# Performance work log

Measured on AMD Instinct MI355X. Metric: run time of the kernel, lower is better.

Reference implementation:

```python
import jax, jax.numpy as jnp
import numpy as np

B, C, H, W = 16, 64, 128, 128
HEADS, DH = 4, 32
HID = HEADS * DH  # 128
EPS = 1e-5


def setup_inputs() -> dict:
    key = jax.random.key(0)
    ks = jax.random.split(key, 3)
    x = jax.random.normal(ks[0], (B, C, H, W), jnp.float32)
    w_qkv = jax.random.normal(ks[1], (3 * HID, C), jnp.float32) * 0.05  # 1x1 conv, no bias
    w_out = jax.random.normal(ks[2], (C, HID), jnp.float32) * 0.05     # 1x1 conv
    b_out = jnp.zeros((C,), jnp.float32)
    gamma = jnp.ones((C,), jnp.float32)   # BatchNorm weight
    beta = jnp.zeros((C,), jnp.float32)   # BatchNorm bias
    return {"x": x, "w_qkv": w_qkv, "w_out": w_out, "b_out": b_out,
            "gamma": gamma, "beta": beta}


def reference(x, w_qkv, w_out, b_out, gamma, beta):
    b, c, h, w = x.shape
    scale = DH ** (-0.5)
    # 1x1 conv to qkv: [b, 3*HID, h, w]
    qkv = jnp.einsum('bcxy,oc->boxy', x, w_qkv)
    q, k, v = jnp.split(qkv, 3, axis=1)

    def rearr(t):  # b (h d) x y -> b h x y d
        return t.reshape(b, HEADS, DH, h, w).transpose(0, 1, 3, 4, 2)

    q, k, v = rearr(q), rearr(k), rearr(v)
    q = jax.nn.softmax(q, axis=-1) * scale  # softmax over feature dim d
    k = jax.nn.softmax(k, axis=-1)
    # linear attention: sum over spatial positions first (O(hw*d*e))
    context = jnp.einsum('bhxyd,bhxye->bhde', k, v)
    out = jnp.einsum('bhde,bhxyd->bhxye', context, q)
    # b h x y e -> b (h e) x y
    out = out.transpose(0, 1, 4, 2, 3).reshape(b, HID, h, w)
    # 1x1 conv out projection
    out = jnp.einsum('bcxy,oc->boxy', out, w_out) + b_out[None, :, None, None]
    # BatchNorm2d (training-mode batch statistics, biased variance, eps=1e-5)
    mean = out.mean(axis=(0, 2, 3), keepdims=True)
    var = ((out - mean) ** 2).mean(axis=(0, 2, 3), keepdims=True)
    out = (out - mean) * jax.lax.rsqrt(var + EPS)
    return out * gamma[None, :, None, None] + beta[None, :, None, None]
```

## Files before the change

kernel.cpp:

```cpp
#include <hip/hip_runtime.h>

typedef __attribute__((ext_vector_type(8))) short bf16x8;
typedef __attribute__((ext_vector_type(4))) float f32x4;

#define SCALEQ 0.17677669529663687f
#define EPSV 1e-5f

__device__ inline unsigned short f2bf(float f) {
  unsigned int u = __float_as_uint(f);
  return (unsigned short)((u + 0x7FFFu + ((u >> 16) & 1u)) >> 16);
}
__device__ inline unsigned int pack2(float a, float b) {
  return (unsigned int)f2bf(a) | ((unsigned int)f2bf(b) << 16);
}

__global__ __launch_bounds__(256) void kwconv(const float* __restrict__ wqkv,
                                              unsigned short* __restrict__ wbf) {
  const int i = blockIdx.x * 256 + threadIdx.x;
  const float4 v = *(const float4*)&wqkv[i * 4];
  *(uint2*)&wbf[i * 4] = make_uint2(pack2(v.x, v.y), pack2(v.z, v.w));
}

__global__ __launch_bounds__(256) void ktr(const float* __restrict__ x,
                                           unsigned short* __restrict__ xsw) {
  __shared__ float xl[64][256];
  const int t = threadIdx.x;
  const int b = blockIdx.x >> 6;
  const int p0 = (blockIdx.x & 63) << 8;
#pragma unroll
  for (int i = 0; i < 16; ++i) {
    int s = i * 256 + t;
    int c = s >> 6, f4 = s & 63;
    float4 v = *(const float4*)&x[((size_t)(b * 64 + c) << 14) + p0 + f4 * 4];
    *(float4*)&xl[c][(f4 * 4) ^ ((c >> 3) << 2)] = v;
  }
  __syncthreads();
#pragma unroll
  for (int i = 0; i < 8; ++i) {
    int a = i * 256 + t;
    int row = a >> 3, gout = a & 7;
    int gsrc = gout ^ (row & 7);
    int col = row ^ (gsrc << 2);
    unsigned int w0 = pack2(xl[gsrc * 8 + 0][col], xl[gsrc * 8 + 1][col]);
    unsigned int w1 = pack2(xl[gsrc * 8 + 2][col], xl[gsrc * 8 + 3][col]);
    unsigned int w2 = pack2(xl[gsrc * 8 + 4][col], xl[gsrc * 8 + 5][col]);
    unsigned int w3 = pack2(xl[gsrc * 8 + 6][col], xl[gsrc * 8 + 7][col]);
    size_t off = ((size_t)(b * 16384 + p0 + row) * 64) + gout * 8;
    *(uint4*)&xsw[off] = make_uint4(w0, w1, w2, w3);
  }
}

__global__ __launch_bounds__(256) void kctx(const unsigned short* __restrict__ xsw,
                                            const unsigned short* __restrict__ wbf,
                                            float* __restrict__ ctx) {
  __shared__ __align__(16) unsigned short kvb[64 * 128];
  const int t = threadIdx.x;
  const int l = t & 63;
  const int w = t >> 6;
  const int b = blockIdx.x >> 6;
  const int pt = blockIdx.x & 63;
  const int lo16 = l & 15, hi4 = l >> 4;

  f32x4 acc2[4];
#pragma unroll
  for (int h = 0; h < 4; ++h) acc2[h] = (f32x4){0.f, 0.f, 0.f, 0.f};

  for (int chunk = 0; chunk < 2; ++chunk) {
    const unsigned short* xb =
        xsw + (size_t)(b * 16384 + pt * 256 + chunk * 128) * 64;
    for (int h = 0; h < 4; ++h) {
      bf16x8 afr[4][2];
#pragma unroll
      for (int Mt = 0; Mt < 4; ++Mt) {
        int row = (Mt < 2) ? (128 + h * 32 + Mt * 16 + lo16)
                           : (256 + h * 32 + (Mt - 2) * 16 + lo16);
#pragma unroll
        for (int Ks = 0; Ks < 2; ++Ks)
          afr[Mt][Ks] = *(const bf16x8*)&wbf[row * 64 + Ks * 32 + (hi4 << 3)];
      }

#pragma unroll
      for (int nt = 0; nt < 2; ++nt) {
        const int p = (w * 2 + nt) * 16 + lo16;
        f32x4 acc[4];
#pragma unroll
        for (int Mt = 0; Mt < 4; ++Mt) acc[Mt] = (f32x4){0.f, 0.f, 0.f, 0.f};
#pragma unroll
        for (int Ks = 0; Ks < 2; ++Ks) {
          int g = Ks * 4 + hi4;
          bf16x8 bfr = *(const bf16x8*)&xb[p * 64 + ((g ^ (p & 7)) << 3)];
#pragma unroll
          for (int Mt = 0; Mt < 4; ++Mt)
            acc[Mt] = __builtin_amdgcn_mfma_f32_16x16x32_bf16(afr[Mt][Ks], bfr,
                                                              acc[Mt], 0, 0, 0);
        }
        float m = acc[0][0];
#pragma unroll
        for (int r = 1; r < 4; ++r) m = fmaxf(m, acc[0][r]);
#pragma unroll
        for (int r = 0; r < 4; ++r) m = fmaxf(m, acc[1][r]);
        m = fmaxf(m, __shfl_xor(m, 16));
        m = fmaxf(m, __shfl_xor(m, 32));
        float s = 0.f;
#pragma unroll
        for (int Mt = 0; Mt < 2; ++Mt)
#pragma unroll
          for (int r = 0; r < 4; ++r) {
            acc[Mt][r] = __expf(acc[Mt][r] - m);
            s += acc[Mt][r];
          }
        s += __shfl_xor(s, 16);
        s += __shfl_xor(s, 32);
        const float inv = 1.f / s;
#pragma unroll
        for (int Mt = 0; Mt < 4; ++Mt) {
#pragma unroll
          for (int r = 0; r < 4; ++r) {
            int row = ((Mt < 2) ? Mt * 16 : 32 + (Mt - 2) * 16) + hi4 * 4 + r;
            float val = (Mt < 2) ? acc[Mt][r] * inv : acc[Mt][r];
            kvb[row * 128 + (((p >> 3) ^ (row & 7)) << 3) + (p & 7)] = f2bf(val);
          }
        }
      }
      __syncthreads();

      const int arow = ((w >> 1) << 4) + lo16;
      const int brow = 32 + ((w & 1) << 4) + lo16;
#pragma unroll
      for (int Ks2 = 0; Ks2 < 4; ++Ks2) {
        int j8 = Ks2 * 4 + hi4;
        bf16x8 ka = *(const bf16x8*)&kvb[arow * 128 + ((j8 ^ (arow & 7)) << 3)];
        bf16x8 va = *(const bf16x8*)&kvb[brow * 128 + ((j8 ^ (brow & 7)) << 3)];
        acc2[h] = __builtin_amdgcn_mfma_f32_16x16x32_bf16(ka, va, acc2[h], 0, 0, 0);
      }
      __syncthreads();
    }
  }

  const int d0 = ((w >> 1) << 4) + hi4 * 4;
  const int e  = ((w & 1) << 4) + lo16;
#pragma unroll
  for (int h = 0; h < 4; ++h)
#pragma unroll
    for (int r = 0; r < 4; ++r)
      atomicAdd(&ctx[(size_t)((b * 4 + h) * 32 + d0 + r) * 32 + e], acc2[h][r]);
}

__global__ __launch_bounds__(256) void kweff(const float* __restrict__ ctx,
                                             const float* __restrict__ wo,
                                             unsigned short* __restrict__ weffbf) {
  __shared__ float ctxl[4 * 1064];
  const int t = threadIdx.x;
  const int b = blockIdx.x;
#pragma unroll
  for (int i = 0; i < 16; ++i) {
    int idx = i * 256 + t;
    int h = idx >> 10, d = (idx >> 5) & 31, e = idx & 31;
    ctxl[h * 1064 + d * 33 + e] = ctx[(size_t)(b * 4 + h) * 1024 + d * 32 + e];
  }
  __syncthreads();
  const int o = t >> 2, h = t & 3;
  float wr[32];
#pragma unroll
  for (int e4 = 0; e4 < 8; ++e4) {
    float4 v = *(const float4*)&wo[o * 128 + h * 32 + e4 * 4];
    wr[e4 * 4] = v.x; wr[e4 * 4 + 1] = v.y;
    wr[e4 * 4 + 2] = v.z; wr[e4 * 4 + 3] = v.w;
  }
  for (int d = 0; d < 32; ++d) {
    float s = 0.f;
#pragma unroll
    for (int e = 0; e < 32; ++e) s = fmaf(wr[e], ctxl[h * 1064 + d * 33 + e], s);
    weffbf[(size_t)b * 8192 + o * 128 + h * 32 + d] = f2bf(s * SCALEQ);
  }
}

__global__ __launch_bounds__(256) void kout(const unsigned short* __restrict__ xsw,
                                            const unsigned short* __restrict__ wbf,
                                            const unsigned short* __restrict__ weffbf,
                                            const float* __restrict__ bo,
                                            float* __restrict__ y,
                                            float* __restrict__ pstats) {
  __shared__ __align__(16) unsigned short xs[128 * 64];
  __shared__ __align__(16) unsigned short qsl[128 * 128];
  const int t = threadIdx.x;
  const int l = t & 63;
  const int w = t >> 6;
  const int b = blockIdx.x >> 7;
  const int p0 = (blockIdx.x & 127) << 7;
  const int lo16 = l & 15, hi4 = l >> 4;
  const unsigned short* web = weffbf + ((size_t)b << 13);

  {
    const uint4* src = (const uint4*)&xsw[(size_t)(b * 16384 + p0) * 64];
    uint4* dst = (uint4*)xs;
#pragma unroll
    for (int i = 0; i < 4; ++i) dst[i * 256 + t] = src[i * 256 + t];
  }
  __syncthreads();

  {
    bf16x8 aq[2][2];
#pragma unroll
    for (int Mt = 0; Mt < 2; ++Mt) {
      int row = w * 32 + Mt * 16 + lo16;
#pragma unroll
      for (int Ks = 0; Ks < 2; ++Ks)
        aq[Mt][Ks] = *(const bf16x8*)&wbf[row * 64 + Ks * 32 + (hi4 << 3)];
    }
#pragma unroll
    for (int Nt = 0; Nt < 8; ++Nt) {
      const int p = Nt * 16 + lo16;
      f32x4 acc[2];
      acc[0] = (f32x4){0.f, 0.f, 0.f, 0.f};
      acc[1] = (f32x4){0.f, 0.f, 0.f, 0.f};
#pragma unroll
      for (int Ks = 0; Ks < 2; ++Ks) {
        int g = Ks * 4 + hi4;
        bf16x8 bfr = *(const bf16x8*)&xs[p * 64 + ((g ^ (p & 7)) << 3)];
#pragma unroll
        for (int Mt = 0; Mt < 2; ++Mt)
          acc[Mt] = __builtin_amdgcn_mfma_f32_16x16x32_bf16(aq[Mt][Ks], bfr,
                                                            acc[Mt], 0, 0, 0);
      }
      float m = acc[0][0];
#pragma unroll
      for (int r = 1; r < 4; ++r) m = fmaxf(m, acc[0][r]);
#pragma unroll
      for (int r = 0; r < 4; ++r) m = fmaxf(m, acc[1][r]);
      m = fmaxf(m, __shfl_xor(m, 16));
      m = fmaxf(m, __shfl_xor(m, 32));
      float s = 0.f;
#pragma unroll
      for (int Mt = 0; Mt < 2; ++Mt)
#pragma unroll
        for (int r = 0; r < 4; ++r) {
          acc[Mt][r] = __expf(acc[Mt][r] - m);
          s += acc[Mt][r];
        }
      s += __shfl_xor(s, 16);
      s += __shfl_xor(s, 32);
      const float inv = 1.f / s;
#pragma unroll
      for (int Mt = 0; Mt < 2; ++Mt) {
#pragma unroll
        for (int pr = 0; pr < 2; ++pr) {
          int hd = w * 32 + Mt * 16 + hi4 * 4 + pr * 2;
          int g = hd >> 3;
          int col = ((g ^ (p & 15)) << 3) | (hd & 7);
          *(unsigned int*)&qsl[p * 128 + col] =
              pack2(acc[Mt][pr * 2] * inv, acc[Mt][pr * 2 + 1] * inv);
        }
      }
    }
  }
  __syncthreads();

  f32x4 accY[2][4];
#pragma unroll
  for (int nt = 0; nt < 2; ++nt)
#pragma unroll
    for (int Mt = 0; Mt < 4; ++Mt) accY[nt][Mt] = (f32x4){0.f, 0.f, 0.f, 0.f};
#pragma unroll
  for (int nt = 0; nt < 2; ++nt) {
    const int p = (w * 2 + nt) * 16 + lo16;
#pragma unroll
    for (int Ks = 0; Ks < 4; ++Ks) {
      int g = Ks * 4 + hi4;
      bf16x8 bq = *(const bf16x8*)&qsl[p * 128 + ((g ^ (p & 15)) << 3)];
#pragma unroll
      for (int Mt = 0; Mt < 4; ++Mt) {
        int o = Mt * 16 + lo16;
        bf16x8 aw = *(const bf16x8*)&web[o * 128 + (g << 3)];
        accY[nt][Mt] = __builtin_amdgcn_mfma_f32_16x16x32_bf16(aw, bq,
                                                               accY[nt][Mt], 0, 0, 0);
      }
    }
  }

  float sacc[16], qacc[16];
#pragma unroll
  for (int i = 0; i < 16; ++i) { sacc[i] = 0.f; qacc[i] = 0.f; }
#pragma unroll
  for (int nt = 0; nt < 2; ++nt) {
    const int p = p0 + (w * 2 + nt) * 16 + lo16;
#pragma unroll
    for (int Mt = 0; Mt < 4; ++Mt) {
#pragma unroll
      for (int r = 0; r < 4; ++r) {
        int o = Mt * 16 + hi4 * 4 + r;
        float val = accY[nt][Mt][r] + bo[o];
        y[((size_t)(b * 64 + o) << 14) + p] = val;
        sacc[Mt * 4 + r] += val;
        qacc[Mt * 4 + r] += val * val;
      }
    }
  }
#pragma unroll
  for (int off = 1; off < 16; off <<= 1) {
#pragma unroll
    for (int i = 0; i < 16; ++i) {
      sacc[i] += __shfl_xor(sacc[i], off);
      qacc[i] += __shfl_xor(qacc[i], off);
    }
  }
  __syncthreads();
  float* red = (float*)qsl;
  if (lo16 == 0) {
#pragma unroll
    for (int i = 0; i < 16; ++i) {
      int o = (i >> 2) * 16 + hi4 * 4 + (i & 3);
      red[w * 128 + o] = sacc[i];
      red[w * 128 + 64 + o] = qacc[i];
    }
  }
  __syncthreads();
  if (t < 128) {
    float s = red[t] + red[128 + t] + red[256 + t] + red[384 + t];
    pstats[(size_t)blockIdx.x * 128 + t] = s;
  }
}

__global__ __launch_bounds__(256) void kred(const float* __restrict__ pstats,
                                            float* __restrict__ ssum,
                                            float* __restrict__ ssq) {
  const int t = threadIdx.x;
  const int which = blockIdx.x >> 6;
  const int o = blockIdx.x & 63;
  const int base = which * 64 + o;
  float s = 0.f;
#pragma unroll
  for (int i = 0; i < 8; ++i)
    s += pstats[(size_t)(i * 256 + t) * 128 + base];
#pragma unroll
  for (int off = 32; off > 0; off >>= 1) s += __shfl_down(s, off);
  __shared__ float ls[4];
  if ((t & 63) == 0) ls[t >> 6] = s;
  __syncthreads();
  if (t == 0) {
    float r = ls[0] + ls[1] + ls[2] + ls[3];
    if (which) ssq[o] = r; else ssum[o] = r;
  }
}

__global__ __launch_bounds__(256) void kbn(float* __restrict__ y,
                                           const float* __restrict__ ssum,
                                           const float* __restrict__ ssq,
                                           const float* __restrict__ gamma,
                                           const float* __restrict__ beta) {
  const int t = threadIdx.x;
  const size_t base = (size_t)blockIdx.x * 8192;
  const int o = (blockIdx.x >> 1) & 63;
  const float invn = 1.f / 262144.f;
  const float mean = ssum[o] * invn;
  const float var = ssq[o] * invn - mean * mean;
  const float g = gamma[o] * rsqrtf(var + EPSV);
  const float sh = beta[o] - mean * g;
#pragma unroll
  for (int it = 0; it < 8; ++it) {
    float4 v = *(float4*)&y[base + it * 1024 + t * 4];
    v.x = v.x * g + sh;
    v.y = v.y * g + sh;
    v.z = v.z * g + sh;
    v.w = v.w * g + sh;
    *(float4*)&y[base + it * 1024 + t * 4] = v;
  }
}

__global__ __launch_bounds__(256) void kctx0(const float* __restrict__ x,
                                             const float* __restrict__ wq,
                                             float* __restrict__ ctxT) {
  __shared__ float kT[32 * 256];
  __shared__ float vT[32 * 256];
  const int t = threadIdx.x;
  const int b = blockIdx.x >> 5;
  const int tile = blockIdx.x & 31;
  const int d0 = (t & 15) << 1;
  const int e0 = (t >> 4) << 1;
  float acc[4][2][2];
#pragma unroll
  for (int h = 0; h < 4; ++h)
#pragma unroll
    for (int i = 0; i < 2; ++i)
#pragma unroll
      for (int j = 0; j < 2; ++j) acc[h][i][j] = 0.f;
  for (int chunk = 0; chunk < 2; ++chunk) {
    const int p = (tile << 9) + (chunk << 8) + t;
    float xr[64];
#pragma unroll
    for (int c = 0; c < 64; ++c) xr[c] = x[((size_t)(b * 64 + c) << 14) + p];
#pragma unroll
    for (int h = 0; h < 4; ++h) {
      float kk[32];
#pragma unroll
      for (int i = 0; i < 32; ++i) {
        const float* wr = wq + (128 + h * 32 + i) * 64;
        float a = 0.f;
#pragma unroll
        for (int c = 0; c < 64; ++c) a = fmaf(wr[c], xr[c], a);
        kk[i] = a;
      }
      float m = kk[0];
#pragma unroll
      for (int i = 1; i < 32; ++i) m = fmaxf(m, kk[i]);
      float s = 0.f;
#pragma unroll
      for (int i = 0; i < 32; ++i) { kk[i] = __expf(kk[i] - m); s += kk[i]; }
      const float inv = 1.f / s;
      float vv[32];
#pragma unroll
      for (int i = 0; i < 32; ++i) {
        const float* wr = wq + (256 + h * 32 + i) * 64;
        float a = 0.f;
#pragma unroll
        for (int c = 0; c < 64; ++c) a = fmaf(wr[c], xr[c], a);
        vv[i] = a;
      }
      __syncthreads();
#pragma unroll
      for (int i = 0; i < 32; ++i) kT[i * 256 + (t ^ (2 * i))] = kk[i] * inv;
#pragma unroll
      for (int i = 0; i < 32; ++i) vT[i * 256 + t] = vv[i];
      __syncthreads();
#pragma unroll 2
      for (int p2 = 0; p2 < 256; p2 += 2) {
        const float2 k0 = *(const float2*)&kT[d0 * 256 + (p2 ^ (2 * d0))];
        const float2 k1 = *(const float2*)&kT[(d0 + 1) * 256 + (p2 ^ (2 * (d0 + 1)))];
        const float2 v0 = *(const float2*)&vT[e0 * 256 + p2];
        const float2 v1 = *(const float2*)&vT[(e0 + 1) * 256 + p2];
        acc[h][0][0] += k0.x * v0.x + k0.y * v0.y;
        acc[h][0][1] += k0.x * v1.x + k0.y * v1.y;
        acc[h][1][0] += k1.x * v0.x + k1.y * v0.y;
        acc[h][1][1] += k1.x * v1.x + k1.y * v1.y;
      }
    }
  }
#pragma unroll
  for (int h = 0; h < 4; ++h)
#pragma unroll
    for (int i = 0; i < 2; ++i)
#pragma unroll
      for (int j = 0; j < 2; ++j)
        atomicAdd(&ctxT[(((b * 4 + h) * 32) + (e0 + j)) * 32 + (d0 + i)],
                  acc[h][i][j]);
}

__global__ __launch_bounds__(256) void kout0(const float* __restrict__ x,
                                             const float* __restrict__ wq,
                                             const float* __restrict__ wo,
                                             const float* __restrict__ bo,
                                             const float* __restrict__ ctxT,
                                             float* __restrict__ y) {
  __shared__ float cl[4096];
  const int t = threadIdx.x;
  const int b = blockIdx.x >> 6;
  const int tile = blockIdx.x & 63;
  const int p = (tile << 8) + t;
#pragma unroll
  for (int i = 0; i < 16; ++i) cl[i * 256 + t] = ctxT[(b << 12) + i * 256 + t];
  __syncthreads();
  float xr[64];
#pragma unroll
  for (int c = 0; c < 64; ++c) xr[c] = x[((size_t)(b * 64 + c) << 14) + p];
  float y0[64];
#pragma unroll
  for (int o = 0; o < 64; ++o) y0[o] = 0.f;
  for (int h = 0; h < 4; ++h) {
    float q[32];
#pragma unroll
    for (int i = 0; i < 32; ++i) {
      const float* wr = wq + (h * 32 + i) * 64;
      float a = 0.f;
#pragma unroll
      for (int c = 0; c < 64; ++c) a = fmaf(wr[c], xr[c], a);
      q[i] = a;
    }
    float m = q[0];
#pragma unroll
    for (int i = 1; i < 32; ++i) m = fmaxf(m, q[i]);
    float s = 0.f;
#pragma unroll
    for (int i = 0; i < 32; ++i) { q[i] = __expf(q[i] - m); s += q[i]; }
    const float inv = SCALEQ / s;
#pragma unroll
    for (int i = 0; i < 32; ++i) q[i] *= inv;
    float oh[32];
#pragma unroll
    for (int e = 0; e < 32; ++e) {
      const float* cr = &cl[(h * 32 + e) * 32];
      float a = 0.f;
#pragma unroll
      for (int d = 0; d < 32; ++d) a = fmaf(cr[d], q[d], a);
      oh[e] = a;
    }
#pragma unroll
    for (int o = 0; o < 64; ++o) {
      const float* wr = wo + o * 128 + h * 32;
      float a = y0[o];
#pragma unroll
      for (int e = 0; e < 32; ++e) a = fmaf(wr[e], oh[e], a);
      y0[o] = a;
    }
  }
#pragma unroll
  for (int o = 0; o < 64; ++o)
    y[((size_t)(b * 64 + o) << 14) + p] = y0[o] + bo[o];
}

__global__ __launch_bounds__(256) void kstats0(const float* __restrict__ y,
                                               float* __restrict__ ssum,
                                               float* __restrict__ ssq) {
  const int t = threadIdx.x;
  const size_t base = (size_t)blockIdx.x * 8192;
  const int o = (blockIdx.x >> 1) & 63;
  float s = 0.f, q = 0.f;
#pragma unroll
  for (int it = 0; it < 8; ++it) {
    const float4 v = *(const float4*)&y[base + it * 1024 + t * 4];
    s += v.x + v.y + v.z + v.w;
    q += v.x * v.x + v.y * v.y + v.z * v.z + v.w * v.w;
  }
#pragma unroll
  for (int off = 32; off > 0; off >>= 1) {
    s += __shfl_down(s, off);
    q += __shfl_down(q, off);
  }
  __shared__ float ls[4], lq[4];
  if ((t & 63) == 0) { ls[t >> 6] = s; lq[t >> 6] = q; }
  __syncthreads();
  if (t == 0) {
    atomicAdd(&ssum[o], ls[0] + ls[1] + ls[2] + ls[3]);
    atomicAdd(&ssq[o], lq[0] + lq[1] + lq[2] + lq[3]);
  }
}

extern "C" void kernel_launch(void* const* d_in, const int* in_sizes, int n_in,
                              void* d_out, int out_size, void* d_ws, size_t ws_size,
                              hipStream_t stream) {
  (void)in_sizes; (void)n_in; (void)out_size;
  const float* x     = (const float*)d_in[0];
  const float* wq    = (const float*)d_in[1];
  const float* wo    = (const float*)d_in[2];
  const float* bo    = (const float*)d_in[3];
  const float* gamma = (const float*)d_in[4];
  const float* beta  = (const float*)d_in[5];
  float* out = (float*)d_out;

  float* ctx  = (float*)d_ws;
  float* ssum = (float*)((char*)d_ws + 262144);
  float* ssq  = (float*)((char*)d_ws + 262400);
  unsigned short* weffbf = (unsigned short*)((char*)d_ws + 262656);
  unsigned short* wbf    = (unsigned short*)((char*)d_ws + 524800);
  float* pstats          = (float*)((char*)d_ws + 573952);
  unsigned short* xsw    = (unsigned short*)((char*)d_ws + 1622528);
  const size_t need = 1622528 + (size_t)16 * 16384 * 64 * 2;

  hipMemsetAsync(d_ws, 0, 262656, stream);
  if (ws_size >= need) {
    kwconv<<<24, 256, 0, stream>>>(wq, wbf);
    ktr<<<1024, 256, 0, stream>>>(x, xsw);
    kctx<<<1024, 256, 0, stream>>>(xsw, wbf, ctx);
    kweff<<<16, 256, 0, stream>>>(ctx, wo, weffbf);
    kout<<<2048, 256, 0, stream>>>(xsw, wbf, weffbf, bo, out, pstats);
    kred<<<128, 256, 0, stream>>>(pstats, ssum, ssq);
    kbn<<<2048, 256, 0, stream>>>(out, ssum, ssq, gamma, beta);
  } else {
    kctx0<<<512, 256, 0, stream>>>(x, wq, ctx);
    kout0<<<1024, 256, 0, stream>>>(x, wq, wo, bo, ctx, out);
    kstats0<<<2048, 256, 0, stream>>>(out, ssum, ssq);
    kbn<<<2048, 256, 0, stream>>>(out, ssum, ssq, gamma, beta);
  }
}
```

Measured before the change: 247.2 us.

## Assign one head per wave in kctx to remove block-wide barriers

The context kernel previously had all four waves cooperate on each head, staging K/V through shared memory and calling __syncthreads twice per head per chunk. Now each wave owns one head, keeps that head's weight fragments in registers once, processes all 256 positions in 64-position chunks, and uses a private shared-memory slice, so block barriers are no longer needed. The trade-off is more registers per wave and a different split of MFMA work across waves.

```diff
diff --git a/kernel.cpp b/kernel.cpp
--- a/kernel.cpp
+++ b/kernel.cpp
@@ -53,97 +53,101 @@
 __global__ __launch_bounds__(256) void kctx(const unsigned short* __restrict__ xsw,
                                             const unsigned short* __restrict__ wbf,
                                             float* __restrict__ ctx) {
-  __shared__ __align__(16) unsigned short kvb[64 * 128];
+  __shared__ __align__(16) unsigned short kvb[4 * 64 * 64];
   const int t = threadIdx.x;
   const int l = t & 63;
   const int w = t >> 6;
   const int b = blockIdx.x >> 6;
   const int pt = blockIdx.x & 63;
   const int lo16 = l & 15, hi4 = l >> 4;
+  unsigned short* kw = kvb + w * 4096;
+  const unsigned short* xb = xsw + (size_t)(b * 16384 + pt * 256) * 64;
+  const int h = w;
+
+  bf16x8 afr[4][2];
+#pragma unroll
+  for (int Mt = 0; Mt < 4; ++Mt) {
+    int row = (Mt < 2) ? (128 + h * 32 + Mt * 16 + lo16)
+                       : (256 + h * 32 + (Mt - 2) * 16 + lo16);
+#pragma unroll
+    for (int Ks = 0; Ks < 2; ++Ks)
+      afr[Mt][Ks] = *(const bf16x8*)&wbf[row * 64 + Ks * 32 + (hi4 << 3)];
+  }
 
   f32x4 acc2[4];
 #pragma unroll
-  for (int h = 0; h < 4; ++h) acc2[h] = (f32x4){0.f, 0.f, 0.f, 0.f};
-
-  for (int chunk = 0; chunk < 2; ++chunk) {
-    const unsigned short* xb =
-        xsw + (size_t)(b * 16384 + pt * 256 + chunk * 128) * 64;
-    for (int h = 0; h < 4; ++h) {
-      bf16x8 afr[4][2];
+  for (int qd = 0; qd < 4; ++qd) acc2[qd] = (f32x4){0.f, 0.f, 0.f, 0.f};
+
+  for (int hc = 0; hc < 4; ++hc) {
+#pragma unroll
+    for (int nt = 0; nt < 4; ++nt) {
+      const int lp = nt * 16 + lo16;
+      const int p = hc * 64 + lp;
+      f32x4 acc[4];
+#pragma unroll
+      for (int Mt = 0; Mt < 4; ++Mt) acc[Mt] = (f32x4){0.f, 0.f, 0.f, 0.f};
+#pragma unroll
+      for (int Ks = 0; Ks < 2; ++Ks) {
+        int g = Ks * 4 + hi4;
+        bf16x8 bfr = *(const bf16x8*)&xb[p * 64 + ((g ^ (p & 7)) << 3)];
+#pragma unroll
+        for (int Mt = 0; Mt < 4; ++Mt)
+          acc[Mt] = __builtin_amdgcn_mfma_f32_16x16x32_bf16(afr[Mt][Ks], bfr,
+                                                            acc[Mt], 0, 0, 0);
+      }
+      float m = acc[0][0];
+#pragma unroll
+      for (int r = 1; r < 4; ++r) m = fmaxf(m, acc[0][r]);
+#pragma unroll
+      for (int r = 0; r < 4; ++r) m = fmaxf(m, acc[1][r]);
+      m = fmaxf(m, __shfl_xor(m, 16));
+      m = fmaxf(m, __shfl_xor(m, 32));
+      float s = 0.f;
+#pragma unroll
+      for (int Mt = 0; Mt < 2; ++Mt)
+#pragma unroll
+        for (int r = 0; r < 4; ++r) {
+          acc[Mt][r] = __expf(acc[Mt][r] - m);
+          s += acc[Mt][r];
+        }
+      s += __shfl_xor(s, 16);
+      s += __shfl_xor(s, 32);
+      const float inv = 1.f / s;
 #pragma unroll
       for (int Mt = 0; Mt < 4; ++Mt) {
-        int row = (Mt < 2) ? (128 + h * 32 + Mt * 16 + lo16)
-                           : (256 + h * 32 + (Mt - 2) * 16 + lo16);
-#pragma unroll
-        for (int Ks = 0; Ks < 2; ++Ks)
-          afr[Mt][Ks] = *(const bf16x8*)&wbf[row * 64 + Ks * 32 + (hi4 << 3)];
-      }
-
-#pragma unroll
-      for (int nt = 0; nt < 2; ++nt) {
-        const int p = (w * 2 + nt) * 16 + lo16;
-        f32x4 acc[4];
-#pragma unroll
-        for (int Mt = 0; Mt < 4; ++Mt) acc[Mt] = (f32x4){0.f, 0.f, 0.f, 0.f};
-#pragma unroll
-        for (int Ks = 0; Ks < 2; ++Ks) {
-          int g = Ks * 4 + hi4;
-          bf16x8 bfr = *(const bf16x8*)&xb[p * 64 + ((g ^ (p & 7)) << 3)];
-#pragma unroll
-          for (int Mt = 0; Mt < 4; ++Mt)
-            acc[Mt] = __builtin_amdgcn_mfma_f32_16x16x32_bf16(afr[Mt][Ks], bfr,
-                                                              acc[Mt], 0, 0, 0);
+#pragma unroll
+        for (int r = 0; r < 4; ++r) {
+          int row = ((Mt < 2) ? Mt * 16 : 32 + (Mt - 2) * 16) + hi4 * 4 + r;
+          float val = (Mt < 2) ? acc[Mt][r] * inv : acc[Mt][r];
+          kw[row * 64 + ((((lp >> 3) ^ (row & 7))) << 3) + (lp & 7)] = f2bf(val);
         }
-        float m = acc[0][0];
-#pragma unroll
-        for (int r = 1; r < 4; ++r) m = fmaxf(m, acc[0][r]);
-#pragma unroll
-        for (int r = 0; r < 4; ++r) m = fmaxf(m, acc[1][r]);
-        m = fmaxf(m, __shfl_xor(m, 16));
-        m = fmaxf(m, __shfl_xor(m, 32));
-        float s = 0.f;
-#pragma unroll
-        for (int Mt = 0; Mt < 2; ++Mt)
-#pragma unroll
-          for (int r = 0; r < 4; ++r) {
-            acc[Mt][r] = __expf(acc[Mt][r] - m);
-            s += acc[Mt][r];
-          }
-        s += __shfl_xor(s, 16);
-        s += __shfl_xor(s, 32);
-        const float inv = 1.f / s;
-#pragma unroll
-        for (int Mt = 0; Mt < 4; ++Mt) {
-#pragma unroll
-          for (int r = 0; r < 4; ++r) {
-            int row = ((Mt < 2) ? Mt * 16 : 32 + (Mt - 2) * 16) + hi4 * 4 + r;
-            float val = (Mt < 2) ? acc[Mt][r] * inv : acc[Mt][r];
-            kvb[row * 128 + (((p >> 3) ^ (row & 7)) << 3) + (p & 7)] = f2bf(val);
-          }
-        }
-      }
-      __syncthreads();
-
-      const int arow = ((w >> 1) << 4) + lo16;
-      const int brow = 32 + ((w & 1) << 4) + lo16;
-#pragma unroll
-      for (int Ks2 = 0; Ks2 < 4; ++Ks2) {
+      }
+    }
+
+#pragma unroll
+    for (int qd = 0; qd < 4; ++qd) {
+      const int arow = ((qd >> 1) << 4) + lo16;
+      const int brow = 32 + ((qd & 1) << 4) + lo16;
+#pragma unroll
+      for (int Ks2 = 0; Ks2 < 2; ++Ks2) {
         int j8 = Ks2 * 4 + hi4;
-        bf16x8 ka = *(const bf16x8*)&kvb[arow * 128 + ((j8 ^ (arow & 7)) << 3)];
-        bf16x8 va = *(const bf16x8*)&kvb[brow * 128 + ((j8 ^ (brow & 7)) << 3)];
-        acc2[h] = __builtin_amdgcn_mfma_f32_16x16x32_bf16(ka, va, acc2[h], 0, 0, 0);
-      }
-      __syncthreads();
-    }
-  }
-
-  const int d0 = ((w >> 1) << 4) + hi4 * 4;
-  const int e  = ((w & 1) << 4) + lo16;
-#pragma unroll
-  for (int h = 0; h < 4; ++h)
+        bf16x8 ka = *(const bf16x8*)&kw[arow * 64 + ((j8 ^ (arow & 7)) << 3)];
+        bf16x8 va = *(const bf16x8*)&kw[brow * 64 + ((j8 ^ (brow & 7)) << 3)];
+        acc2[qd] = __builtin_amdgcn_mfma_f32_16x16x32_bf16(ka, va, acc2[qd],
+                                                           0, 0, 0);
+      }
+    }
+  }
+
+#pragma unroll
+  for (int qd = 0; qd < 4; ++qd) {
+    const int d0 = ((qd >> 1) << 4) + hi4 * 4;
+    const int e  = ((qd & 1) << 4) + lo16;
 #pragma unroll
     for (int r = 0; r < 4; ++r)
-      atomicAdd(&ctx[(size_t)((b * 4 + h) * 32 + d0 + r) * 32 + e], acc2[h][r]);
+      atomicAdd(&ctx[(size_t)((b * 4 + h) * 32 + d0 + r) * 32 + e],
+                acc2[qd][r]);
+  }
 }
 
 __global__ __launch_bounds__(256) void kweff(const float* __restrict__ ctx,
```

Measured after the change: 234.1 us. 5.3% less time.
